# Performance work log

Measured on AMD Instinct MI355X. Metric: run time of the kernel, lower is better.

Reference implementation:

```python
import jax, jax.numpy as jnp
import numpy as np

KK = 9  # 3x3 kernel points
PAD = 1
EPS = 1e-5


def _conv2d(x, w, b):
    # x: [B,C,H,W], w: [O,I,3,3]
    y = jax.lax.conv_general_dilated(
        x, w, window_strides=(1, 1), padding=((PAD, PAD), (PAD, PAD)),
        dimension_numbers=("NCHW", "OIHW", "NCHW"))
    return y + b[None, :, None, None]


def _bilinear_sample_one(img, py, px):
    # img: [C,H,W]; py, px: [KK,H,W] fractional sample coords
    C, H, W = img.shape
    y0 = jnp.floor(py).astype(jnp.int32)
    x0 = jnp.floor(px).astype(jnp.int32)
    wy = py - y0
    wx = px - x0

    def g(yi, xi):
        ok = ((yi >= 0) & (yi < H) & (xi >= 0) & (xi < W)).astype(img.dtype)
        v = img[:, jnp.clip(yi, 0, H - 1), jnp.clip(xi, 0, W - 1)]  # [C,KK,H,W]
        return v * ok[None]

    v00 = g(y0, x0)
    v01 = g(y0, x0 + 1)
    v10 = g(y0 + 1, x0)
    v11 = g(y0 + 1, x0 + 1)
    return (v00 * (1 - wy) * (1 - wx) + v01 * (1 - wy) * wx
            + v10 * wy * (1 - wx) + v11 * wy * wx)  # [C,KK,H,W]


def setup_inputs() -> dict:
    key = jax.random.key(0)
    ks = jax.random.split(key, 8)
    B, C, H, W = 8, 256, 96, 96
    O = 256
    x = jax.random.normal(ks[0], (B, C, H, W), dtype=jnp.float32)
    # modulated DCNv2 offset/mask conv: 3*KK output channels
    w_off = jax.random.normal(ks[1], (3 * KK, C, 3, 3), dtype=jnp.float32) * 0.01
    b_off = jnp.zeros((3 * KK,), dtype=jnp.float32)
    w_dcn = jax.random.normal(ks[2], (O, C, 3, 3), dtype=jnp.float32) * (1.0 / np.sqrt(C * KK))
    b_dcn = jnp.zeros((O,), dtype=jnp.float32)
    gamma = jnp.ones((O,), dtype=jnp.float32)
    beta = jnp.zeros((O,), dtype=jnp.float32)
    running_mean = jax.random.normal(ks[3], (O,), dtype=jnp.float32) * 0.1
    running_var = jax.random.uniform(ks[4], (O,), dtype=jnp.float32, minval=0.5, maxval=1.5)
    return {"x": x, "w_off": w_off, "b_off": b_off, "w_dcn": w_dcn,
            "b_dcn": b_dcn, "gamma": gamma, "beta": beta,
            "running_mean": running_mean, "running_var": running_var}


def reference(x, w_off, b_off, w_dcn, b_dcn, gamma, beta, running_mean, running_var):
    B, C, H, W = x.shape
    O = w_dcn.shape[0]
    # offsets + modulation masks
    om = _conv2d(x, w_off, b_off)                  # [B, 3*KK, H, W]
    offset = om[:, :2 * KK]
    mask = jax.nn.sigmoid(om[:, 2 * KK:])          # [B, KK, H, W]
    off_y = offset[:, 0::2]                        # [B, KK, H, W]
    off_x = offset[:, 1::2]

    ky, kx = jnp.meshgrid(jnp.arange(3), jnp.arange(3), indexing="ij")
    ky = ky.reshape(KK).astype(x.dtype)
    kx = kx.reshape(KK).astype(x.dtype)
    hh = jnp.arange(H, dtype=x.dtype)
    ww = jnp.arange(W, dtype=x.dtype)
    # fractional sampling coordinates per output pixel per kernel point
    py = off_y + hh[None, None, :, None] + ky[None, :, None, None] - PAD
    px = off_x + ww[None, None, None, :] + kx[None, :, None, None] - PAD

    sampled = jax.vmap(_bilinear_sample_one)(x, py, px)  # [B,C,KK,H,W]
    sampled = sampled * mask[:, None]
    out = jnp.einsum("bckhw,ock->bohw", sampled, w_dcn.reshape(O, C, KK))
    out = out + b_dcn[None, :, None, None]
    # BatchNorm (inference, running stats) + ReLU
    inv = jax.lax.rsqrt(running_var + EPS)
    out = (out - running_mean[None, :, None, None]) * (gamma * inv)[None, :, None, None]
    out = out + beta[None, :, None, None]
    return jax.nn.relu(out)
```

## Files before the change

kernel.cpp:

```cpp
#include <hip/hip_runtime.h>
#include <hip/hip_bf16.h>
#include <hip/hip_fp16.h>
#include <cstdint>
#include <cstddef>

#define H 96
#define W 96
#define HW 9216
#define C 256
#define B 8
#define O 256
#define KK 9
#define EPS 1e-5f

typedef __attribute__((ext_vector_type(8))) short short8;
typedef __attribute__((ext_vector_type(4))) float float4v;
typedef __attribute__((ext_vector_type(2))) float float2v;
typedef unsigned short ushort_t;
typedef unsigned int uint_t;

__global__ __launch_bounds__(256) void transpose_x_k(
    const float* __restrict__ x, ushort_t* __restrict__ xt)
{
    __shared__ float tile[64][65];
    int t = threadIdx.x;
    int p0 = blockIdx.x * 64;
    int c0 = blockIdx.y * 64;
    int b  = blockIdx.z;
    {
        int tx = t & 63, ty = t >> 6;
        const float* xb = x + ((size_t)b * C + c0 + ty) * HW + p0 + tx;
#pragma unroll
        for (int i = 0; i < 64; i += 4)
            tile[ty + i][tx] = xb[(size_t)i * HW];
    }
    __syncthreads();
    {
        int tc = t & 31, tp = t >> 5;
        ushort_t* xtb = xt + ((size_t)b * HW + p0) * C + c0;
#pragma unroll
        for (int i = 0; i < 64; i += 8) {
            int p = tp + i;
            float a  = tile[2 * tc][p];
            float bb = tile[2 * tc + 1][p];
            __hip_bfloat162 h2 = __float22bfloat162_rn(make_float2(a, bb));
            uint_t u;
            __builtin_memcpy(&u, &h2, 4);
            *reinterpret_cast<uint_t*>(&xtb[(size_t)p * C + 2 * tc]) = u;
        }
    }
}

__global__ __launch_bounds__(256) void prep_w_k(
    const float* __restrict__ wd, const float* __restrict__ wo,
    ushort_t* __restrict__ bp, ushort_t* __restrict__ bo)
{
    int idx = blockIdx.x * 256 + threadIdx.x;
    if (idx < KK * O * C) {
        int kk = idx / (O * C);
        int r = idx - kk * O * C;
        int o = r >> 8, c = r & 255;
        float v = wd[((size_t)o * C + c) * KK + kk];
        __hip_bfloat16 hh = __float2bfloat16(v);
        ushort_t u;
        __builtin_memcpy(&u, &hh, 2);
        bp[idx] = u;
    } else {
        int j = idx - KK * O * C;
        int n = j / (KK * C);
        int r = j - n * KK * C;
        int kk = r >> 8, c = r & 255;
        float v = (n < 27) ? wo[((size_t)n * C + c) * KK + kk] : 0.0f;
        __hip_bfloat16 hh = __float2bfloat16(v);
        ushort_t u;
        __builtin_memcpy(&u, &hh, 2);
        bo[j] = u;
    }
}

__global__ __launch_bounds__(256) void offset_mfma_k(
    const ushort_t* __restrict__ xt, const ushort_t* __restrict__ bo,
    const float* __restrict__ b_off, float* __restrict__ om)
{
    int t = threadIdx.x;
    int wv = t >> 6, l = t & 63;
    int ln = l & 15, lq = l >> 4;
    int d = blockIdx.x;
    int lb = (d & 7) * 144 + (d >> 3);
    int p0 = lb * 64;
    int b = p0 / HW;
    int rem0w = p0 - b * HW + wv * 16;
    const ushort_t* xtb = xt + (size_t)b * HW * C;

    int rem = rem0w + ln;
    int hh0 = rem / W;
    int ww0 = rem - hh0 * W;

    float4v acc[2];
    acc[0] = (float4v){0.f, 0.f, 0.f, 0.f};
    acc[1] = (float4v){0.f, 0.f, 0.f, 0.f};

#pragma unroll
    for (int kk = 0; kk < KK; ++kk) {
        int dy = kk / 3 - 1, dx = kk % 3 - 1;
        int hh = hh0 + dy, ww = ww0 + dx;
        bool ok = (hh >= 0) & (hh < H) & (ww >= 0) & (ww < W);
        uint_t msk = ok ? 0xffffffffu : 0u;
        int hc = min(max(hh, 0), H - 1);
        int wc = min(max(ww, 0), W - 1);
        const ushort_t* ap = xtb + (size_t)(hc * W + wc) * C + lq * 8;
        const ushort_t* bp0 = bo + ((size_t)(0 * 16 + ln) * KK + kk) * C + lq * 8;
        const ushort_t* bp1 = bo + ((size_t)(1 * 16 + ln) * KK + kk) * C + lq * 8;
#pragma unroll
        for (int cc = 0; cc < 8; ++cc) {
            int c0 = cc * 32;
            uint4 u = *(const uint4*)(ap + c0);
            u.x &= msk; u.y &= msk; u.z &= msk; u.w &= msk;
            short8 af;
            __builtin_memcpy(&af, &u, 16);
            short8 bf0 = *(const short8*)(bp0 + c0);
            short8 bf1 = *(const short8*)(bp1 + c0);
            acc[0] = __builtin_amdgcn_mfma_f32_16x16x32_bf16(af, bf0, acc[0], 0, 0, 0);
            acc[1] = __builtin_amdgcn_mfma_f32_16x16x32_bf16(af, bf1, acc[1], 0, 0, 0);
        }
    }

    float* omb = om + (size_t)b * 27 * HW + rem0w;
#pragma unroll
    for (int nt = 0; nt < 2; ++nt) {
        int oc = nt * 16 + ln;
        if (oc < 27) {
            float bv = b_off[oc];
            float* po = omb + (size_t)oc * HW + lq * 4;
            float4 v;
            v.x = acc[nt].x + bv;
            v.y = acc[nt].y + bv;
            v.z = acc[nt].z + bv;
            v.w = acc[nt].w + bv;
            *(float4*)po = v;
        }
    }
}

__device__ __forceinline__ float2v up2(uint_t u) {
    float2v r;
    r.x = __uint_as_float(u << 16);
    r.y = __uint_as_float(u & 0xffff0000u);
    return r;
}

__device__ __forceinline__ uint_t packbf2(float a, float b) {
    __hip_bfloat162 h2 = __float22bfloat162_rn(make_float2(a, b));
    uint_t u;
    __builtin_memcpy(&u, &h2, 4);
    return u;
}

__global__ __launch_bounds__(256) void dcn_main_k(
    const ushort_t* __restrict__ xt, const float* __restrict__ om,
    const ushort_t* __restrict__ bp, const float* __restrict__ b_dcn,
    const float* __restrict__ gamma, const float* __restrict__ beta,
    const float* __restrict__ rmean, const float* __restrict__ rvar,
    float* __restrict__ out)
{
    __shared__ uint3    s_rec[64 * KK];
    __shared__ ushort_t s_a[2][4][64][32];

    int t = threadIdx.x;
    int d = blockIdx.x;
    int lb = (d & 7) * 144 + (d >> 3);
    int p0 = lb * 64;
    int b = p0 / HW;
    int rem0 = p0 - b * HW;

    for (int v = t; v < 64 * KK; v += 256) {
        int m = v & 63;
        int k = v >> 6;
        int rem = rem0 + m;
        int h = rem / W;
        int w = rem - h * W;
        const float* omb = om + (size_t)b * 27 * HW + rem;
        float offy = omb[(size_t)(2 * k) * HW];
        float offx = omb[(size_t)(2 * k + 1) * HW];
        float z    = omb[(size_t)(18 + k) * HW];
        float mval = 1.0f / (1.0f + __expf(-z));
        float py = (float)(h + k / 3 - 1) + offy;
        float px = (float)(w + k % 3 - 1) + offx;
        float fy = floorf(py), fx = floorf(px);
        int y0 = (int)fy, x0 = (int)fx;
        float wy = py - fy, wx = px - fx;
        float row0f = (1.0f - wy) * mval * ((y0 >= 0 && y0 < H) ? 1.0f : 0.0f);
        float row1f = wy * mval * ((y0 >= -1 && y0 < H - 1) ? 1.0f : 0.0f);
        int xsel = min(max(x0, 0), W - 2);
        float wxa = (x0 >= 0 && x0 < W) ? (1.0f - wx) : 0.0f;
        float wxb = (x0 >= -1 && x0 < W - 1) ? wx : 0.0f;
        int cx0 = min(max(x0, 0), W - 1);
        int cx1 = min(max(x0 + 1, 0), W - 1);
        float wA = ((cx0 == xsel) ? wxa : 0.0f) + ((cx1 == xsel) ? wxb : 0.0f);
        float wB = ((cx0 == xsel + 1) ? wxa : 0.0f) + ((cx1 == xsel + 1) ? wxb : 0.0f);
        int yc0 = min(max(y0, 0), H - 1);
        int yc1 = min(max(y0 + 1, 0), H - 1);
        uint3 rr;
        rr.x = (uint_t)(yc0 * W + xsel) | ((uint_t)(yc1 * W + xsel) << 16);
        __half2 h01 = __floats2half2_rn(row0f, row1f);
        __half2 hAB = __floats2half2_rn(wA, wB);
        __builtin_memcpy(&rr.y, &h01, 4);
        __builtin_memcpy(&rr.z, &hAB, 4);
        s_rec[v] = rr;
    }

    float4v acc[4][4];
#pragma unroll
    for (int i = 0; i < 4; ++i)
#pragma unroll
        for (int j = 0; j < 4; ++j)
            acc[i][j] = (float4v){0.f, 0.f, 0.f, 0.f};

    const ushort_t* xtb = xt + (size_t)b * HW * C;
    int wv = t >> 6;
    int l  = t & 63;
    int ln = l & 15;
    int lq = l >> 4;
    int sm = t >> 2;
    int sc = (t & 3) * 8;

    __syncthreads();

#define DECREC(rr_, cb_, a0_, a1_, Wt_) do {                                \
        int px0_ = (rr_).x & 0xffff;                                        \
        int px1_ = (rr_).x >> 16;                                           \
        (a0_) = xtb + (size_t)px0_ * C + (cb_) + sc;                        \
        (a1_) = xtb + (size_t)px1_ * C + (cb_) + sc;                        \
        __half2 h01_, hAB_;                                                 \
        __builtin_memcpy(&h01_, &(rr_).y, 4);                               \
        __builtin_memcpy(&hAB_, &(rr_).z, 4);                               \
        float r0_ = __low2float(h01_), r1_ = __high2float(h01_);            \
        float wa_ = __low2float(hAB_), wb_ = __high2float(hAB_);            \
        (Wt_)[0] = r0_ * wa_; (Wt_)[1] = r0_ * wb_;                         \
        (Wt_)[2] = r1_ * wa_; (Wt_)[3] = r1_ * wb_;                         \
    } while (0)

#define COMBINE(L0_, L1_, L2_, L3_, W_, dst_) do {                          \
        uint4 pk_;                                                          \
        float2v r0_ = up2((L0_).x) * (W_)[0] + up2((L1_).x) * (W_)[1]       \
                    + up2((L2_).x) * (W_)[2] + up2((L3_).x) * (W_)[3];      \
        float2v r1_ = up2((L0_).y) * (W_)[0] + up2((L1_).y) * (W_)[1]       \
                    + up2((L2_).y) * (W_)[2] + up2((L3_).y) * (W_)[3];      \
        float2v r2_ = up2((L0_).z) * (W_)[0] + up2((L1_).z) * (W_)[1]       \
                    + up2((L2_).z) * (W_)[2] + up2((L3_).z) * (W_)[3];      \
        float2v r3_ = up2((L0_).w) * (W_)[0] + up2((L1_).w) * (W_)[1]       \
                    + up2((L2_).w) * (W_)[2] + up2((L3_).w) * (W_)[3];      \
        pk_.x = packbf2(r0_.x, r0_.y);                                      \
        pk_.y = packbf2(r1_.x, r1_.y);                                      \
        pk_.z = packbf2(r2_.x, r2_.y);                                      \
        pk_.w = packbf2(r3_.x, r3_.y);                                      \
        *(uint4*)(dst_) = pk_;                                              \
    } while (0)

    {
        uint3 rr = s_rec[sm];
        const ushort_t *a0, *a1;
        float Wt[4];
        DECREC(rr, 0, a0, a1, Wt);
#pragma unroll
        for (int ci = 0; ci < 4; ++ci) {
            uint4 L0 = *(const uint4*)(a0 + ci * 32);
            uint4 L1 = *(const uint4*)(a0 + ci * 32 + C);
            uint4 L2 = *(const uint4*)(a1 + ci * 32);
            uint4 L3 = *(const uint4*)(a1 + ci * 32 + C);
            COMBINE(L0, L1, L2, L3, Wt, &s_a[0][ci][sm][sc]);
        }
    }
    __syncthreads();

    for (int ph = 0; ph < 2 * KK; ++ph) {
        int rb = ph & 1;
        int wb = rb ^ 1;
        bool more = (ph < 2 * KK - 1);
        int tap = ph >> 1, hf = ph & 1;

        const ushort_t* a0n = xtb;
        const ushort_t* a1n = xtb;
        float Wn[4] = {0.f, 0.f, 0.f, 0.f};
        if (more) {
            int np = ph + 1;
            uint3 rr = s_rec[(np >> 1) * 64 + sm];
            DECREC(rr, (np & 1) * 128, a0n, a1n, Wn);
        }

        const ushort_t* bpk = bp + ((size_t)tap * O + wv * 64 + ln) * C + hf * 128 + lq * 8;
        short8 bfr[4], bfrN[4];
#pragma unroll
        for (int nt = 0; nt < 4; ++nt)
            bfr[nt] = *(const short8*)(bpk + (size_t)nt * 16 * C);

#pragma unroll
        for (int ci = 0; ci < 4; ++ci) {
            uint4 L0, L1, L2, L3;
            if (more) {
                L0 = *(const uint4*)(a0n + ci * 32);
                L1 = *(const uint4*)(a0n + ci * 32 + C);
                L2 = *(const uint4*)(a1n + ci * 32);
                L3 = *(const uint4*)(a1n + ci * 32 + C);
            }
            if (ci < 3) {
#pragma unroll
                for (int nt = 0; nt < 4; ++nt)
                    bfrN[nt] = *(const short8*)(bpk + (size_t)nt * 16 * C + (ci + 1) * 32);
            }
            short8 af[4];
#pragma unroll
            for (int mt = 0; mt < 4; ++mt)
                af[mt] = *(const short8*)&s_a[rb][ci][mt * 16 + ln][lq * 8];
#pragma unroll
            for (int mt = 0; mt < 4; ++mt)
#pragma unroll
                for (int nt = 0; nt < 4; ++nt)
                    acc[mt][nt] = __builtin_amdgcn_mfma_f32_16x16x32_bf16(
                        af[mt], bfr[nt], acc[mt][nt], 0, 0, 0);
            if (more)
                COMBINE(L0, L1, L2, L3, Wn, &s_a[wb][ci][sm][sc]);
#pragma unroll
            for (int nt = 0; nt < 4; ++nt)
                bfr[nt] = bfrN[nt];
        }
        __syncthreads();
    }
#undef COMBINE
#undef DECREC

#pragma unroll
    for (int nt = 0; nt < 4; ++nt) {
        int o = wv * 64 + nt * 16 + ln;
        float scale = gamma[o] * rsqrtf(rvar[o] + EPS);
        float shift = (b_dcn[o] - rmean[o]) * scale + beta[o];
        float* po = out + ((size_t)b * O + o) * HW + rem0 + lq * 4;
#pragma unroll
        for (int mt = 0; mt < 4; ++mt) {
            float4 vv;
            vv.x = fmaxf(acc[mt][nt].x * scale + shift, 0.0f);
            vv.y = fmaxf(acc[mt][nt].y * scale + shift, 0.0f);
            vv.z = fmaxf(acc[mt][nt].z * scale + shift, 0.0f);
            vv.w = fmaxf(acc[mt][nt].w * scale + shift, 0.0f);
            *(float4*)(po + mt * 16) = vv;
        }
    }
}

extern "C" void kernel_launch(void* const* d_in, const int* in_sizes, int n_in,
                              void* d_out, int out_size, void* d_ws, size_t ws_size,
                              hipStream_t stream) {
    const float* x     = (const float*)d_in[0];
    const float* w_off = (const float*)d_in[1];
    const float* b_off = (const float*)d_in[2];
    const float* w_dcn = (const float*)d_in[3];
    const float* b_dcn = (const float*)d_in[4];
    const float* gamma = (const float*)d_in[5];
    const float* beta  = (const float*)d_in[6];
    const float* rmean = (const float*)d_in[7];
    const float* rvar  = (const float*)d_in[8];
    float* out = (float*)d_out;

    float*    om  = (float*)d_ws;
    ushort_t* bpw = (ushort_t*)(om + (size_t)B * 27 * HW);
    ushort_t* bow = bpw + (size_t)KK * O * C;
    ushort_t* xtw = bow + (size_t)32 * KK * C;

    hipLaunchKernelGGL(transpose_x_k, dim3(144, 4, 8), dim3(256), 0, stream,
                       x, xtw);
    hipLaunchKernelGGL(prep_w_k, dim3((KK * O * C + 32 * KK * C) / 256), dim3(256),
                       0, stream, w_dcn, w_off, bpw, bow);
    hipLaunchKernelGGL(offset_mfma_k, dim3(73728 / 64), dim3(256), 0, stream,
                       xtw, bow, b_off, om);
    hipLaunchKernelGGL(dcn_main_k, dim3(73728 / 64), dim3(256), 0, stream,
                       xtw, om, bpw, b_dcn, gamma, beta, rmean, rvar, out);
}
```

Before: 489.0 us.

## Fuse offset conv into main DCN kernel and swizzle shared A tile

The offset/mask MFMA convolution moves into dcn_main_k, and its 27x64 results are staged in shared memory (aliasing s_a) instead of a global om buffer. This removes one kernel launch and the global write and read-back of offsets. The LDS A-tile column index is also XOR-swizzled on both the write and the read side to reduce bank conflicts. In exchange, each block does the offset GEMM serially before its main loop, which lengthens the prologue and may raise register pressure.

```diff
diff --git a/kernel.cpp b/kernel.cpp
--- a/kernel.cpp
+++ b/kernel.cpp
@@ -78,70 +78,6 @@
     }
 }
 
-__global__ __launch_bounds__(256) void offset_mfma_k(
-    const ushort_t* __restrict__ xt, const ushort_t* __restrict__ bo,
-    const float* __restrict__ b_off, float* __restrict__ om)
-{
-    int t = threadIdx.x;
-    int wv = t >> 6, l = t & 63;
-    int ln = l & 15, lq = l >> 4;
-    int d = blockIdx.x;
-    int lb = (d & 7) * 144 + (d >> 3);
-    int p0 = lb * 64;
-    int b = p0 / HW;
-    int rem0w = p0 - b * HW + wv * 16;
-    const ushort_t* xtb = xt + (size_t)b * HW * C;
-
-    int rem = rem0w + ln;
-    int hh0 = rem / W;
-    int ww0 = rem - hh0 * W;
-
-    float4v acc[2];
-    acc[0] = (float4v){0.f, 0.f, 0.f, 0.f};
-    acc[1] = (float4v){0.f, 0.f, 0.f, 0.f};
-
-#pragma unroll
-    for (int kk = 0; kk < KK; ++kk) {
-        int dy = kk / 3 - 1, dx = kk % 3 - 1;
-        int hh = hh0 + dy, ww = ww0 + dx;
-        bool ok = (hh >= 0) & (hh < H) & (ww >= 0) & (ww < W);
-        uint_t msk = ok ? 0xffffffffu : 0u;
-        int hc = min(max(hh, 0), H - 1);
-        int wc = min(max(ww, 0), W - 1);
-        const ushort_t* ap = xtb + (size_t)(hc * W + wc) * C + lq * 8;
-        const ushort_t* bp0 = bo + ((size_t)(0 * 16 + ln) * KK + kk) * C + lq * 8;
-        const ushort_t* bp1 = bo + ((size_t)(1 * 16 + ln) * KK + kk) * C + lq * 8;
-#pragma unroll
-        for (int cc = 0; cc < 8; ++cc) {
-            int c0 = cc * 32;
-            uint4 u = *(const uint4*)(ap + c0);
-            u.x &= msk; u.y &= msk; u.z &= msk; u.w &= msk;
-            short8 af;
-            __builtin_memcpy(&af, &u, 16);
-            short8 bf0 = *(const short8*)(bp0 + c0);
-            short8 bf1 = *(const short8*)(bp1 + c0);
-            acc[0] = __builtin_amdgcn_mfma_f32_16x16x32_bf16(af, bf0, acc[0], 0, 0, 0);
-            acc[1] = __builtin_amdgcn_mfma_f32_16x16x32_bf16(af, bf1, acc[1], 0, 0, 0);
-        }
-    }
-
-    float* omb = om + (size_t)b * 27 * HW + rem0w;
-#pragma unroll
-    for (int nt = 0; nt < 2; ++nt) {
-        int oc = nt * 16 + ln;
-        if (oc < 27) {
-            float bv = b_off[oc];
-            float* po = omb + (size_t)oc * HW + lq * 4;
-            float4 v;
-            v.x = acc[nt].x + bv;
-            v.y = acc[nt].y + bv;
-            v.z = acc[nt].z + bv;
-            v.w = acc[nt].w + bv;
-            *(float4*)po = v;
-        }
-    }
-}
-
 __device__ __forceinline__ float2v up2(uint_t u) {
     float2v r;
     r.x = __uint_as_float(u << 16);
@@ -157,8 +93,9 @@
 }
 
 __global__ __launch_bounds__(256) void dcn_main_k(
-    const ushort_t* __restrict__ xt, const float* __restrict__ om,
-    const ushort_t* __restrict__ bp, const float* __restrict__ b_dcn,
+    const ushort_t* __restrict__ xt, const ushort_t* __restrict__ bo,
+    const ushort_t* __restrict__ bp, const float* __restrict__ b_off,
+    const float* __restrict__ b_dcn,
     const float* __restrict__ gamma, const float* __restrict__ beta,
     const float* __restrict__ rmean, const float* __restrict__ rvar,
     float* __restrict__ out)
@@ -172,49 +109,6 @@
     int p0 = lb * 64;
     int b = p0 / HW;
     int rem0 = p0 - b * HW;
-
-    for (int v = t; v < 64 * KK; v += 256) {
-        int m = v & 63;
-        int k = v >> 6;
-        int rem = rem0 + m;
-        int h = rem / W;
-        int w = rem - h * W;
-        const float* omb = om + (size_t)b * 27 * HW + rem;
-        float offy = omb[(size_t)(2 * k) * HW];
-        float offx = omb[(size_t)(2 * k + 1) * HW];
-        float z    = omb[(size_t)(18 + k) * HW];
-        float mval = 1.0f / (1.0f + __expf(-z));
-        float py = (float)(h + k / 3 - 1) + offy;
-        float px = (float)(w + k % 3 - 1) + offx;
-        float fy = floorf(py), fx = floorf(px);
-        int y0 = (int)fy, x0 = (int)fx;
-        float wy = py - fy, wx = px - fx;
-        float row0f = (1.0f - wy) * mval * ((y0 >= 0 && y0 < H) ? 1.0f : 0.0f);
-        float row1f = wy * mval * ((y0 >= -1 && y0 < H - 1) ? 1.0f : 0.0f);
-        int xsel = min(max(x0, 0), W - 2);
-        float wxa = (x0 >= 0 && x0 < W) ? (1.0f - wx) : 0.0f;
-        float wxb = (x0 >= -1 && x0 < W - 1) ? wx : 0.0f;
-        int cx0 = min(max(x0, 0), W - 1);
-        int cx1 = min(max(x0 + 1, 0), W - 1);
-        float wA = ((cx0 == xsel) ? wxa : 0.0f) + ((cx1 == xsel) ? wxb : 0.0f);
-        float wB = ((cx0 == xsel + 1) ? wxa : 0.0f) + ((cx1 == xsel + 1) ? wxb : 0.0f);
-        int yc0 = min(max(y0, 0), H - 1);
-        int yc1 = min(max(y0 + 1, 0), H - 1);
-        uint3 rr;
-        rr.x = (uint_t)(yc0 * W + xsel) | ((uint_t)(yc1 * W + xsel) << 16);
-        __half2 h01 = __floats2half2_rn(row0f, row1f);
-        __half2 hAB = __floats2half2_rn(wA, wB);
-        __builtin_memcpy(&rr.y, &h01, 4);
-        __builtin_memcpy(&rr.z, &hAB, 4);
-        s_rec[v] = rr;
-    }
-
-    float4v acc[4][4];
-#pragma unroll
-    for (int i = 0; i < 4; ++i)
-#pragma unroll
-        for (int j = 0; j < 4; ++j)
-            acc[i][j] = (float4v){0.f, 0.f, 0.f, 0.f};
 
     const ushort_t* xtb = xt + (size_t)b * HW * C;
     int wv = t >> 6;
@@ -223,6 +117,100 @@
     int lq = l >> 4;
     int sm = t >> 2;
     int sc = (t & 3) * 8;
+    int scw = sc ^ ((sm & 6) << 2);
+    int lqw = (lq * 8) ^ ((ln & 6) << 2);
+
+    {
+        float* s_om = (float*)s_a;
+        int rem_w = rem0 + wv * 16 + ln;
+        int hh0 = rem_w / W;
+        int ww0 = rem_w - hh0 * W;
+        float4v oacc[2];
+        oacc[0] = (float4v){0.f, 0.f, 0.f, 0.f};
+        oacc[1] = (float4v){0.f, 0.f, 0.f, 0.f};
+#pragma unroll
+        for (int kk = 0; kk < KK; ++kk) {
+            int dy = kk / 3 - 1, dx = kk % 3 - 1;
+            int hh = hh0 + dy, ww = ww0 + dx;
+            bool ok = (hh >= 0) & (hh < H) & (ww >= 0) & (ww < W);
+            uint_t msk = ok ? 0xffffffffu : 0u;
+            int hc = min(max(hh, 0), H - 1);
+            int wc = min(max(ww, 0), W - 1);
+            const ushort_t* ap = xtb + (size_t)(hc * W + wc) * C + lq * 8;
+            const ushort_t* bp0 = bo + ((size_t)(0 * 16 + ln) * KK + kk) * C + lq * 8;
+            const ushort_t* bp1 = bo + ((size_t)(1 * 16 + ln) * KK + kk) * C + lq * 8;
+#pragma unroll
+            for (int cc = 0; cc < 8; ++cc) {
+                int c0 = cc * 32;
+                uint4 u = *(const uint4*)(ap + c0);
+                u.x &= msk; u.y &= msk; u.z &= msk; u.w &= msk;
+                short8 af;
+                __builtin_memcpy(&af, &u, 16);
+                short8 bf0 = *(const short8*)(bp0 + c0);
+                short8 bf1 = *(const short8*)(bp1 + c0);
+                oacc[0] = __builtin_amdgcn_mfma_f32_16x16x32_bf16(af, bf0, oacc[0], 0, 0, 0);
+                oacc[1] = __builtin_amdgcn_mfma_f32_16x16x32_bf16(af, bf1, oacc[1], 0, 0, 0);
+            }
+        }
+#pragma unroll
+        for (int nt = 0; nt < 2; ++nt) {
+            int oc = nt * 16 + ln;
+            if (oc < 27) {
+                float bv = b_off[oc];
+                int px = wv * 16 + lq * 4;
+                s_om[oc * 64 + px + 0] = oacc[nt].x + bv;
+                s_om[oc * 64 + px + 1] = oacc[nt].y + bv;
+                s_om[oc * 64 + px + 2] = oacc[nt].z + bv;
+                s_om[oc * 64 + px + 3] = oacc[nt].w + bv;
+            }
+        }
+    }
+    __syncthreads();
+
+    {
+        const float* s_om = (const float*)s_a;
+        for (int v = t; v < 64 * KK; v += 256) {
+            int m = v & 63;
+            int k = v >> 6;
+            int rem = rem0 + m;
+            int h = rem / W;
+            int w = rem - h * W;
+            float offy = s_om[(2 * k) * 64 + m];
+            float offx = s_om[(2 * k + 1) * 64 + m];
+            float z    = s_om[(18 + k) * 64 + m];
+            float mval = 1.0f / (1.0f + __expf(-z));
+            float py = (float)(h + k / 3 - 1) + offy;
+            float px = (float)(w + k % 3 - 1) + offx;
+            float fy = floorf(py), fx = floorf(px);
+            int y0 = (int)fy, x0 = (int)fx;
+            float wy = py - fy, wx = px - fx;
+            float row0f = (1.0f - wy) * mval * ((y0 >= 0 && y0 < H) ? 1.0f : 0.0f);
+            float row1f = wy * mval * ((y0 >= -1 && y0 < H - 1) ? 1.0f : 0.0f);
+            int xsel = min(max(x0, 0), W - 2);
+            float wxa = (x0 >= 0 && x0 < W) ? (1.0f - wx) : 0.0f;
+            float wxb = (x0 >= -1 && x0 < W - 1) ? wx : 0.0f;
+            int cx0 = min(max(x0, 0), W - 1);
+            int cx1 = min(max(x0 + 1, 0), W - 1);
+            float wA = ((cx0 == xsel) ? wxa : 0.0f) + ((cx1 == xsel) ? wxb : 0.0f);
+            float wB = ((cx0 == xsel + 1) ? wxa : 0.0f) + ((cx1 == xsel + 1) ? wxb : 0.0f);
+            int yc0 = min(max(y0, 0), H - 1);
+            int yc1 = min(max(y0 + 1, 0), H - 1);
+            uint3 rr;
+            rr.x = (uint_t)(yc0 * W + xsel) | ((uint_t)(yc1 * W + xsel) << 16);
+            __half2 h01 = __floats2half2_rn(row0f, row1f);
+            __half2 hAB = __floats2half2_rn(wA, wB);
+            __builtin_memcpy(&rr.y, &h01, 4);
+            __builtin_memcpy(&rr.z, &hAB, 4);
+            s_rec[v] = rr;
+        }
+    }
+
+    float4v acc[4][4];
+#pragma unroll
+    for (int i = 0; i < 4; ++i)
+#pragma unroll
+        for (int j = 0; j < 4; ++j)
+            acc[i][j] = (float4v){0.f, 0.f, 0.f, 0.f};
 
     __syncthreads();
 
@@ -268,7 +256,7 @@
             uint4 L1 = *(const uint4*)(a0 + ci * 32 + C);
             uint4 L2 = *(const uint4*)(a1 + ci * 32);
             uint4 L3 = *(const uint4*)(a1 + ci * 32 + C);
-            COMBINE(L0, L1, L2, L3, Wt, &s_a[0][ci][sm][sc]);
+            COMBINE(L0, L1, L2, L3, Wt, &s_a[0][ci][sm][scw]);
         }
     }
     __syncthreads();
@@ -311,7 +299,7 @@
             short8 af[4];
 #pragma unroll
             for (int mt = 0; mt < 4; ++mt)
-                af[mt] = *(const short8*)&s_a[rb][ci][mt * 16 + ln][lq * 8];
+                af[mt] = *(const short8*)&s_a[rb][ci][mt * 16 + ln][lqw];
 #pragma unroll
             for (int mt = 0; mt < 4; ++mt)
 #pragma unroll
@@ -319,7 +307,7 @@
                     acc[mt][nt] = __builtin_amdgcn_mfma_f32_16x16x32_bf16(
                         af[mt], bfr[nt], acc[mt][nt], 0, 0, 0);
             if (more)
-                COMBINE(L0, L1, L2, L3, Wn, &s_a[wb][ci][sm][sc]);
+                COMBINE(L0, L1, L2, L3, Wn, &s_a[wb][ci][sm][scw]);
 #pragma unroll
             for (int nt = 0; nt < 4; ++nt)
                 bfr[nt] = bfrN[nt];
@@ -361,8 +349,7 @@
     const float* rvar  = (const float*)d_in[8];
     float* out = (float*)d_out;
 
-    float*    om  = (float*)d_ws;
-    ushort_t* bpw = (ushort_t*)(om + (size_t)B * 27 * HW);
+    ushort_t* bpw = (ushort_t*)d_ws;
     ushort_t* bow = bpw + (size_t)KK * O * C;
     ushort_t* xtw = bow + (size_t)32 * KK * C;
 
@@ -370,8 +357,6 @@
                        x, xtw);
     hipLaunchKernelGGL(prep_w_k, dim3((KK * O * C + 32 * KK * C) / 256), dim3(256),
                        0, stream, w_dcn, w_off, bpw, bow);
-    hipLaunchKernelGGL(offset_mfma_k, dim3(73728 / 64), dim3(256), 0, stream,
-                       xtw, bow, b_off, om);
     hipLaunchKernelGGL(dcn_main_k, dim3(73728 / 64), dim3(256), 0, stream,
-                       xtw, om, bpw, b_dcn, gamma, beta, rmean, rvar, out);
-}
+                       xtw, bow, bpw, b_off, b_dcn, gamma, beta, rmean, rvar, out);
+}
```

Measured after the change: 482.5 us. No clear change (-1.3%).
